# Performance work log

Hardware: AMD Instinct MI355X
Metric: run time of the kernel (lower is better)

The kernel has to match this reference:

```python
import jax, jax.numpy as jnp
import numpy as np

H = 1024   # hidden_size
NH = 16    # num_heads
HD = H // NH
B, S = 2, 2048


def setup_inputs() -> dict:
    key = jax.random.key(0)
    ks = jax.random.split(key, 6)
    std = 0.02
    x = jax.random.normal(ks[0], (B, S, H), dtype=jnp.float32)
    w_qkv = jax.random.normal(ks[1], (3 * H, H), dtype=jnp.float32) * std
    b_qkv = jnp.zeros((3 * H,), dtype=jnp.float32)
    ln_g = jnp.ones((H,), dtype=jnp.float32)
    ln_b = jnp.zeros((H,), dtype=jnp.float32)
    w_ent = jax.random.normal(ks[2], (1, H), dtype=jnp.float32) * std
    b_ent = jnp.zeros((1,), dtype=jnp.float32)
    w_out = jax.random.normal(ks[3], (H, H), dtype=jnp.float32) * std
    b_out = jnp.zeros((H,), dtype=jnp.float32)
    return {"x": x, "ln_g": ln_g, "ln_b": ln_b, "w_qkv": w_qkv, "b_qkv": b_qkv,
            "w_ent": w_ent, "b_ent": b_ent, "w_out": w_out, "b_out": b_out}


def reference(x, ln_g, ln_b, w_qkv, b_qkv, w_ent, b_ent, w_out, b_out):
    b, s, h = x.shape
    scale = 1.0 / jnp.sqrt(jnp.float32(HD))
    TEMP = 0.1  # fixed softmax temperature

    # LayerNorm (eps=1e-6)
    mu = jnp.mean(x, axis=-1, keepdims=True)
    var = jnp.mean(jnp.square(x - mu), axis=-1, keepdims=True)
    xn = (x - mu) / jnp.sqrt(var + 1e-6) * ln_g + ln_b

    # QKV projection -> [B, S, 3, NH, HD] -> q,k,v each [B, NH, S, HD]
    qkv = xn @ w_qkv.T + b_qkv
    qkv = qkv.reshape(b, s, 3, NH, HD).transpose(2, 0, 3, 1, 4)
    q, k, v = qkv[0], qkv[1], qkv[2]

    # Scaled causal scores [B, NH, S, S]
    scores = jnp.einsum('bhqd,bhkd->bhqk', q, k) * scale
    causal = jnp.tril(jnp.ones((s, s), dtype=bool))
    scores = jnp.where(causal[None, None], scores, -jnp.inf)

    # Sharpened softmax (temperature 0.1); dropout is identity in eval
    probs = jax.nn.softmax(scores / TEMP, axis=-1)

    # Entropy gate over keys: sigmoid proj on post-LN x, clamped [0.1, 2.0]
    gate = jax.nn.sigmoid(xn @ w_ent.T + b_ent)        # [B, S, 1]
    gate = jnp.clip(gate, 0.1, 2.0)[:, None, None, :, 0]  # [B, 1, 1, S]
    probs = probs * gate

    # Weighted values -> merge heads -> output projection, scaled by 0.1
    out = jnp.einsum('bhqk,bhkd->bhqd', probs, v)
    out = out.transpose(0, 2, 1, 3).reshape(b, s, h)
    return (out @ w_out.T + b_out) * 0.1
```

## Files before the change

### kernel.cpp

```cpp
#include <hip/hip_runtime.h>

typedef __bf16 bf16x8 __attribute__((ext_vector_type(8)));
typedef float floatx4 __attribute__((ext_vector_type(4)));
typedef unsigned short u16;

#define LOG2E 1.44269504088896340736f
#define BF16_ONE 0x3F80u

static __device__ __forceinline__ float bf2f(u16 u) {
  union { unsigned int i; float f; } c; c.i = ((unsigned int)u) << 16; return c.f;
}
static __device__ __forceinline__ u16 f2bf(float f) {
  union { float f; unsigned int i; } c; c.f = f;
  unsigned int x = c.i;
  unsigned int r = (x >> 16) & 1u;
  x += 0x7fffu + r;
  return (u16)(x >> 16);
}
static __device__ __forceinline__ u16 f2bf_rne(float f) {
  __bf16 h = (__bf16)f;
  union { __bf16 h; u16 u; } c; c.h = h; return c.u;
}
static __device__ __forceinline__ float fast_exp2(float x) {
#if __has_builtin(__builtin_amdgcn_exp2f)
  return __builtin_amdgcn_exp2f(x);
#else
  return exp2f(x);
#endif
}
static __device__ __forceinline__ float ldp(const void* p, int i, bool isbf) {
  return isbf ? bf2f(((const u16*)p)[i]) : ((const float*)p)[i];
}

static __device__ __forceinline__ float blockSum(float v, float* red, int wave, int lane) {
  #pragma unroll
  for (int o = 32; o > 0; o >>= 1) v += __shfl_xor(v, o);
  __syncthreads();
  if (lane == 0) red[wave] = v;
  __syncthreads();
  return red[0] + red[1] + red[2] + red[3];
}

__global__ __launch_bounds__(256) void prep_kernel(
    const void* __restrict__ w_qkv, u16* __restrict__ w_qkv_c,
    const void* __restrict__ w_out, u16* __restrict__ w_out_c,
    const void* __restrict__ x, const void* __restrict__ g, const void* __restrict__ bta,
    const void* __restrict__ w_ent, const void* __restrict__ b_ent,
    u16* __restrict__ xn, float* __restrict__ gate, const u16* __restrict__ probe)
{
  __shared__ float red[4];
  bool isbf = (probe[0] == BF16_ONE);
  int blk = blockIdx.x;
  int tid = threadIdx.x;

  if (blk < 2048) {
    int i = blk * 256 + tid;
    const void* src = w_qkv; u16* dst = w_qkv_c;
    if (i >= 393216) { i -= 393216; src = w_out; dst = w_out_c; }
    if (isbf) {
      ((uint4*)dst)[i] = ((const uint4*)src)[i];
    } else {
      const float4* s = (const float4*)src;
      float4 a = s[2 * i], b = s[2 * i + 1];
      u16 o[8] = {f2bf(a.x), f2bf(a.y), f2bf(a.z), f2bf(a.w),
                  f2bf(b.x), f2bf(b.y), f2bf(b.z), f2bf(b.w)};
      *(uint4*)(&dst[8 * i]) = *(uint4*)o;
    }
    return;
  }

  int row = blk - 2048;
  int wave = tid >> 6, lane = tid & 63;

  float v[4];
  #pragma unroll
  for (int i = 0; i < 4; ++i) {
    size_t idx = (size_t)row * 1024 + tid + 256 * i;
    v[i] = isbf ? bf2f(((const u16*)x)[idx]) : ((const float*)x)[idx];
  }

  float mu = blockSum(v[0] + v[1] + v[2] + v[3], red, wave, lane) * (1.0f / 1024.0f);

  float vs = 0.f;
  #pragma unroll
  for (int i = 0; i < 4; ++i) { float d = v[i] - mu; vs += d * d; }
  float var = blockSum(vs, red, wave, lane) * (1.0f / 1024.0f);
  float rstd = rsqrtf(var + 1e-6f);

  float gp = 0.f;
  #pragma unroll
  for (int i = 0; i < 4; ++i) {
    int col = tid + 256 * i;
    float xv = (v[i] - mu) * rstd * ldp(g, col, isbf) + ldp(bta, col, isbf);
    xn[(size_t)row * 1024 + col] = f2bf(xv);
    gp += xv * ldp(w_ent, col, isbf);
  }
  float tot = blockSum(gp, red, wave, lane);
  if (tid == 0) {
    float z = tot + ldp(b_ent, 0, isbf);
    float sg = 1.0f / (1.0f + exp2f(-z * LOG2E));
    gate[row] = fminf(fmaxf(sg, 0.1f), 2.0f);
  }
}

#define GEMM_STAGE(Abase, Wbase) \
  { \
    int lrow = lane >> 3; \
    int scb = ((lane & 7) ^ lrow) * 8; \
    _Pragma("unroll") \
    for (int it = 0; it < 4; ++it) { \
      int chunk = wave * 4 + it; \
      int row = chunk * 8 + lrow; \
      __builtin_amdgcn_global_load_lds( \
        (const __attribute__((address_space(1))) void*)&Abase[(size_t)(m0 + row) * K + k0 + scb], \
        (__attribute__((address_space(3))) void*)&As[chunk * 512], 16, 0, 0); \
      __builtin_amdgcn_global_load_lds( \
        (const __attribute__((address_space(1))) void*)&Wbase[(size_t)(n0 + row) * K + k0 + scb], \
        (__attribute__((address_space(3))) void*)&Ws[chunk * 512], 16, 0, 0); \
    } \
  }

#define GEMM_COMPUTE() \
  _Pragma("unroll") \
  for (int kk = 0; kk < 64; kk += 32) { \
    int kkb = kk >> 3; \
    bf16x8 af[4], bfr[4]; \
    _Pragma("unroll") \
    for (int i = 0; i < 4; ++i) \
      af[i] = *(const bf16x8*)(&As[(wm + 16 * i + lr) * 64 + ((kkb + lg) ^ (lr & 7)) * 8]); \
    _Pragma("unroll") \
    for (int j = 0; j < 4; ++j) \
      bfr[j] = *(const bf16x8*)(&Ws[(wn + 16 * j + lr) * 64 + ((kkb + lg) ^ (lr & 7)) * 8]); \
    _Pragma("unroll") \
    for (int i = 0; i < 4; ++i) \
      _Pragma("unroll") \
      for (int j = 0; j < 4; ++j) \
        acc[i][j] = __builtin_amdgcn_mfma_f32_16x16x32_bf16(af[i], bfr[j], acc[i][j], 0, 0, 0); \
  }

__global__ __launch_bounds__(256) void gemm_bt_kernel(
    const u16* __restrict__ A, const u16* __restrict__ W, const void* __restrict__ bias,
    const float* __restrict__ gate, u16* __restrict__ C, int M, int N, int K,
    const u16* __restrict__ probe)
{
  __shared__ __align__(16) u16 As[128 * 64];
  __shared__ __align__(16) u16 Ws[128 * 64];
  int m0 = blockIdx.y * 128, n0 = blockIdx.x * 128;
  int tid = threadIdx.x, wave = tid >> 6, lane = tid & 63;
  int lr = lane & 15, lg = lane >> 4;
  int wm = (wave >> 1) * 64, wn = (wave & 1) * 64;

  floatx4 acc[4][4];
  #pragma unroll
  for (int i = 0; i < 4; ++i)
    #pragma unroll
    for (int j = 0; j < 4; ++j)
      #pragma unroll
      for (int r = 0; r < 4; ++r) acc[i][j][r] = 0.f;

  for (int k0 = 0; k0 < K; k0 += 64) {
    GEMM_STAGE(A, W)
    __syncthreads();
    GEMM_COMPUTE()
    __syncthreads();
  }

  bool isbf = (probe[0] == BF16_ONE);
  bool doGate = (n0 >= 2048);
  float gm[4][4];
  #pragma unroll
  for (int i = 0; i < 4; ++i)
    #pragma unroll
    for (int r = 0; r < 4; ++r)
      gm[i][r] = doGate ? gate[m0 + wm + 16 * i + lg * 4 + r] : 1.0f;

  #pragma unroll
  for (int j = 0; j < 4; ++j) {
    int n = n0 + wn + 16 * j + lr;
    float bv = ldp(bias, n, isbf);
    #pragma unroll
    for (int i = 0; i < 4; ++i) {
      int mbase = m0 + wm + 16 * i + lg * 4;
      #pragma unroll
      for (int r = 0; r < 4; ++r)
        C[(size_t)(mbase + r) * N + n] = f2bf((acc[i][j][r] + bv) * gm[i][r]);
    }
  }
}

__global__ __launch_bounds__(256) void gemm_out_kernel(
    const u16* __restrict__ A, const u16* __restrict__ W, const void* __restrict__ bias,
    void* __restrict__ C, int M, int N, int K, float scale, const u16* __restrict__ probe)
{
  __shared__ __align__(16) u16 As[64 * 64];
  __shared__ __align__(16) u16 Ws[128 * 64];
  int m0 = blockIdx.y * 64, n0 = blockIdx.x * 128;
  int tid = threadIdx.x, wave = tid >> 6, lane = tid & 63;
  int lr = lane & 15, lg = lane >> 4;
  int wn = wave * 32;

  floatx4 acc[4][2];
  #pragma unroll
  for (int i = 0; i < 4; ++i)
    #pragma unroll
    for (int j = 0; j < 2; ++j)
      #pragma unroll
      for (int r = 0; r < 4; ++r) acc[i][j][r] = 0.f;

  for (int k0 = 0; k0 < K; k0 += 64) {
    {
      int lrow = lane >> 3;
      int scb = ((lane & 7) ^ lrow) * 8;
      #pragma unroll
      for (int c = wave; c < 24; c += 4) {
        if (c < 8) {
          int row = c * 8 + lrow;
          __builtin_amdgcn_global_load_lds(
            (const __attribute__((address_space(1))) void*)&A[(size_t)(m0 + row) * K + k0 + scb],
            (__attribute__((address_space(3))) void*)&As[c * 512], 16, 0, 0);
        } else {
          int cc = c - 8;
          int row = cc * 8 + lrow;
          __builtin_amdgcn_global_load_lds(
            (const __attribute__((address_space(1))) void*)&W[(size_t)(n0 + row) * K + k0 + scb],
            (__attribute__((address_space(3))) void*)&Ws[cc * 512], 16, 0, 0);
        }
      }
    }
    __syncthreads();
    #pragma unroll
    for (int kk = 0; kk < 64; kk += 32) {
      int kkb = kk >> 3;
      bf16x8 af[4], bfr[2];
      #pragma unroll
      for (int i = 0; i < 4; ++i)
        af[i] = *(const bf16x8*)(&As[(16 * i + lr) * 64 + ((kkb + lg) ^ (lr & 7)) * 8]);
      #pragma unroll
      for (int j = 0; j < 2; ++j)
        bfr[j] = *(const bf16x8*)(&Ws[(wn + 16 * j + lr) * 64 + ((kkb + lg) ^ (lr & 7)) * 8]);
      #pragma unroll
      for (int i = 0; i < 4; ++i)
        #pragma unroll
        for (int j = 0; j < 2; ++j)
          acc[i][j] = __builtin_amdgcn_mfma_f32_16x16x32_bf16(af[i], bfr[j], acc[i][j], 0, 0, 0);
    }
    __syncthreads();
  }

  bool isbf = (probe[0] == BF16_ONE);
  #pragma unroll
  for (int j = 0; j < 2; ++j) {
    int n = n0 + wn + 16 * j + lr;
    float bv = ldp(bias, n, isbf);
    #pragma unroll
    for (int i = 0; i < 4; ++i) {
      int mbase = m0 + 16 * i + lg * 4;
      #pragma unroll
      for (int r = 0; r < 4; ++r) {
        float v = (acc[i][j][r] + bv) * scale;
        size_t idx = (size_t)(mbase + r) * N + n;
        if (isbf) ((u16*)C)[idx] = f2bf(v);
        else      ((float*)C)[idx] = v;
      }
    }
  }
}

#define PSTR 72
#define CEXP (1.25f * LOG2E)

__global__ __launch_bounds__(512, 4) void attn_kernel(
    const u16* __restrict__ qkv, u16* __restrict__ out)
{
  __shared__ __align__(16) u16 Ks[2][64 * 72];
  __shared__ __align__(16) u16 Vt[2][64 * 72];
  __shared__ __align__(16) u16 Ps[8][16 * PSTR];

  int bid = blockIdx.x;
  int xcd = bid & 7, kb = bid >> 3;
  int bh = xcd * 4 + (kb >> 4);
  int pr = kb & 15;
  int h = bh & 15, b = bh >> 4;
  int tid = threadIdx.x, wave = tid >> 6, lane = tid & 63;
  int lr = lane & 15, lg = lane >> 4;
  const int RS = 3072;

  int tA = pr, tB = 31 - pr;
  bool isA = (wave >= 4);
  int wv = wave & 3;
  int myT = isA ? tA : tB;

  bf16x8 qf[2];
  int qrb = b * 2048 + myT * 64 + wv * 16;
  #pragma unroll
  for (int kk = 0; kk < 2; ++kk)
    qf[kk] = *(const bf16x8*)(&qkv[(size_t)(qrb + lr) * RS + h * 64 + kk * 32 + lg * 8]);

  floatx4 accO[4];
  float l = 0.f;
  #pragma unroll
  for (int jt = 0; jt < 4; ++jt)
    #pragma unroll
    for (int r = 0; r < 4; ++r) accO[jt][r] = 0.f;

  u16* ps = Ps[wave];

  int srow = tid >> 3, sc8 = (tid & 7) * 8;
  int kq = tid & 31, dg = tid >> 5;
  uint4 kp;
  uint2 vv0, vv1;

  auto LOADKV = [&](int kt) {
    int krow0 = b * 2048 + kt * 64;
    kp = *(const uint4*)(&qkv[(size_t)(krow0 + srow) * RS + 1024 + h * 64 + sc8]);
    const u16* vbp = &qkv[(size_t)krow0 * RS + 2048 + h * 64];
    vv0 = *(const uint2*)(&vbp[(size_t)(2 * kq) * RS + 4 * dg]);
    vv1 = *(const uint2*)(&vbp[(size_t)(2 * kq + 1) * RS + 4 * dg]);
  };
  auto COMMIT = [&](int bi) {
    *(uint4*)(&Ks[bi][srow * 72 + sc8]) = kp;
    #pragma unroll
    for (int d = 0; d < 4; ++d) {
      unsigned w0 = (&vv0.x)[d >> 1], w1 = (&vv1.x)[d >> 1];
      unsigned e0 = (d & 1) ? (w0 >> 16) : (w0 & 0xffffu);
      unsigned e1 = (d & 1) ? (w1 >> 16) : (w1 & 0xffffu);
      *(unsigned*)(&Vt[bi][(4 * dg + d) * 72 + 2 * kq]) = e0 | (e1 << 16);
    }
  };

  LOADKV(0);
  COMMIT(0);
  LOADKV(1);
  __syncthreads();

  int qg = wv * 16 + lr;
  for (int kt = 0; kt <= tB; ++kt) {
    int cur = kt & 1;
    if (!isA || kt <= tA) {
      bool diag = (kt == myT);
      const u16* ks = Ks[cur];
      const u16* vt = Vt[cur];
      #pragma unroll
      for (int jt = 0; jt < 4; ++jt) {
        floatx4 a = {0.f, 0.f, 0.f, 0.f};
        #pragma unroll
        for (int kk = 0; kk < 2; ++kk) {
          bf16x8 bk = *(const bf16x8*)(&ks[(jt * 16 + lr) * 72 + kk * 32 + lg * 8]);
          a = __builtin_amdgcn_mfma_f32_16x16x32_bf16(bk, qf[kk], a, 0, 0, 0);
        }
        int kbase = jt * 16 + lg * 4;
        u16 pb[4];
        #pragma unroll
        for (int r = 0; r < 4; ++r) {
          float e = fast_exp2(a[r] * CEXP);
          if (diag && (kbase + r) > qg) e = 0.f;
          l += e;
          pb[r] = f2bf_rne(e);
        }
        *(uint2*)(&ps[lr * PSTR + kbase]) = *(uint2*)pb;
      }
      bf16x8 ap[2];
      #pragma unroll
      for (int kk = 0; kk < 2; ++kk)
        ap[kk] = *(const bf16x8*)(&ps[lr * PSTR + kk * 32 + lg * 8]);
      #pragma unroll
      for (int jt = 0; jt < 4; ++jt)
        #pragma unroll
        for (int kk = 0; kk < 2; ++kk) {
          bf16x8 bv = *(const bf16x8*)(&vt[(jt * 16 + lr) * 72 + kk * 32 + lg * 8]);
          accO[jt] = __builtin_amdgcn_mfma_f32_16x16x32_bf16(ap[kk], bv, accO[jt], 0, 0, 0);
        }
    }
    if (kt < tB) {
      COMMIT(cur ^ 1);
      if (kt + 2 <= tB) LOADKV(kt + 2);
      __syncthreads();
    }
  }

  l += __shfl_xor(l, 16); l += __shfl_xor(l, 32);
  float li[4];
  #pragma unroll
  for (int r = 0; r < 4; ++r)
    li[r] = 1.0f / fmaxf(__shfl(l, lg * 4 + r), 1e-30f);
  #pragma unroll
  for (int jt = 0; jt < 4; ++jt)
    #pragma unroll
    for (int r = 0; r < 4; ++r) {
      int m = qrb + lg * 4 + r;
      out[(size_t)m * 1024 + h * 64 + jt * 16 + lr] = f2bf(accO[jt][r] * li[r]);
    }
}

extern "C" void kernel_launch(void* const* d_in, const int* in_sizes, int n_in,
                              void* d_out, int out_size, void* d_ws, size_t ws_size,
                              hipStream_t stream) {
  const void* x     = d_in[0];
  const void* ln_g  = d_in[1];
  const void* ln_b  = d_in[2];
  const void* w_qkv = d_in[3];
  const void* b_qkv = d_in[4];
  const void* w_ent = d_in[5];
  const void* b_ent = d_in[6];
  const void* w_out = d_in[7];
  const void* b_out = d_in[8];
  const u16* probe = (const u16*)ln_g;

  char* ws = (char*)d_ws;
  float* gate    = (float*)(ws);
  u16* xc        = (u16*)(ws + (64u << 10));
  u16* qkvb      = (u16*)(ws + (64u << 10) + (8u << 20));
  u16* w_qkv_c   = (u16*)(ws + (64u << 10) + (32u << 20));
  u16* w_out_c   = (u16*)(ws + (64u << 10) + (38u << 20));

  prep_kernel<<<6144, 256, 0, stream>>>(w_qkv, w_qkv_c, w_out, w_out_c,
                                        x, ln_g, ln_b, w_ent, b_ent, xc, gate, probe);
  gemm_bt_kernel<<<dim3(24, 32), 256, 0, stream>>>(xc, w_qkv_c, b_qkv, gate, qkvb, 4096, 3072, 1024, probe);
  attn_kernel<<<512, 512, 0, stream>>>(qkvb, xc );
  gemm_out_kernel<<<dim3(8, 64), 256, 0, stream>>>(xc, w_out_c, b_out, d_out, 4096, 1024, 1024, 0.1f, probe);
}
```

Baseline: 199.0 us.

## Retile QKV GEMM to 128x192 with 512 threads and skip bf16 weight copy

The QKV projection GEMM now uses 128x192 tiles across 8 waves, with each wave computing a 64x48 sub-tile. This gives 512 blocks, which should fill the CUs more evenly than the old 768 blocks of 128x128. When inputs are already bf16, the prep kernel skips copying the weights and both GEMMs read the original weight buffers directly. The gate multiply is now chosen per 16-column sub-tile, because a 192-wide tile can straddle the V boundary at 2048.

```diff
diff --git a/kernel.cpp b/kernel.cpp
--- a/kernel.cpp
+++ b/kernel.cpp
@@ -54,18 +54,15 @@
   int tid = threadIdx.x;
 
   if (blk < 2048) {
+    if (isbf) return;
     int i = blk * 256 + tid;
     const void* src = w_qkv; u16* dst = w_qkv_c;
     if (i >= 393216) { i -= 393216; src = w_out; dst = w_out_c; }
-    if (isbf) {
-      ((uint4*)dst)[i] = ((const uint4*)src)[i];
-    } else {
-      const float4* s = (const float4*)src;
-      float4 a = s[2 * i], b = s[2 * i + 1];
-      u16 o[8] = {f2bf(a.x), f2bf(a.y), f2bf(a.z), f2bf(a.w),
-                  f2bf(b.x), f2bf(b.y), f2bf(b.z), f2bf(b.w)};
-      *(uint4*)(&dst[8 * i]) = *(uint4*)o;
-    }
+    const float4* s = (const float4*)src;
+    float4 a = s[2 * i], b = s[2 * i + 1];
+    u16 o[8] = {f2bf(a.x), f2bf(a.y), f2bf(a.z), f2bf(a.w),
+                f2bf(b.x), f2bf(b.y), f2bf(b.z), f2bf(b.w)};
+    *(uint4*)(&dst[8 * i]) = *(uint4*)o;
     return;
   }
 
@@ -103,97 +100,104 @@
   }
 }
 
-#define GEMM_STAGE(Abase, Wbase) \
-  { \
-    int lrow = lane >> 3; \
-    int scb = ((lane & 7) ^ lrow) * 8; \
-    _Pragma("unroll") \
-    for (int it = 0; it < 4; ++it) { \
-      int chunk = wave * 4 + it; \
-      int row = chunk * 8 + lrow; \
-      __builtin_amdgcn_global_load_lds( \
-        (const __attribute__((address_space(1))) void*)&Abase[(size_t)(m0 + row) * K + k0 + scb], \
-        (__attribute__((address_space(3))) void*)&As[chunk * 512], 16, 0, 0); \
-      __builtin_amdgcn_global_load_lds( \
-        (const __attribute__((address_space(1))) void*)&Wbase[(size_t)(n0 + row) * K + k0 + scb], \
-        (__attribute__((address_space(3))) void*)&Ws[chunk * 512], 16, 0, 0); \
-    } \
-  }
-
-#define GEMM_COMPUTE() \
-  _Pragma("unroll") \
-  for (int kk = 0; kk < 64; kk += 32) { \
-    int kkb = kk >> 3; \
-    bf16x8 af[4], bfr[4]; \
-    _Pragma("unroll") \
-    for (int i = 0; i < 4; ++i) \
-      af[i] = *(const bf16x8*)(&As[(wm + 16 * i + lr) * 64 + ((kkb + lg) ^ (lr & 7)) * 8]); \
-    _Pragma("unroll") \
-    for (int j = 0; j < 4; ++j) \
-      bfr[j] = *(const bf16x8*)(&Ws[(wn + 16 * j + lr) * 64 + ((kkb + lg) ^ (lr & 7)) * 8]); \
-    _Pragma("unroll") \
-    for (int i = 0; i < 4; ++i) \
-      _Pragma("unroll") \
-      for (int j = 0; j < 4; ++j) \
-        acc[i][j] = __builtin_amdgcn_mfma_f32_16x16x32_bf16(af[i], bfr[j], acc[i][j], 0, 0, 0); \
-  }
-
-__global__ __launch_bounds__(256) void gemm_bt_kernel(
-    const u16* __restrict__ A, const u16* __restrict__ W, const void* __restrict__ bias,
-    const float* __restrict__ gate, u16* __restrict__ C, int M, int N, int K,
+__global__ __launch_bounds__(512, 4) void gemm_qkv_kernel(
+    const u16* __restrict__ A, const void* __restrict__ Wf, const u16* __restrict__ Wc,
+    const void* __restrict__ bias, const float* __restrict__ gate, u16* __restrict__ C,
     const u16* __restrict__ probe)
 {
   __shared__ __align__(16) u16 As[128 * 64];
-  __shared__ __align__(16) u16 Ws[128 * 64];
-  int m0 = blockIdx.y * 128, n0 = blockIdx.x * 128;
+  __shared__ __align__(16) u16 Ws[192 * 64];
+  const int K = 1024, N = 3072;
+  bool isbf = (probe[0] == BF16_ONE);
+  const u16* W = isbf ? (const u16*)Wf : Wc;
+
+  int bid = blockIdx.x;
+  int n0 = (bid & 15) * 192, m0 = (bid >> 4) * 128;
   int tid = threadIdx.x, wave = tid >> 6, lane = tid & 63;
   int lr = lane & 15, lg = lane >> 4;
-  int wm = (wave >> 1) * 64, wn = (wave & 1) * 64;
-
-  floatx4 acc[4][4];
+  int wm = (wave >> 2) * 64, wn = (wave & 3) * 48;
+  int lrow = lane >> 3;
+  int scb = ((lane & 7) ^ lrow) * 8;
+
+  floatx4 acc[4][3];
   #pragma unroll
   for (int i = 0; i < 4; ++i)
     #pragma unroll
-    for (int j = 0; j < 4; ++j)
+    for (int j = 0; j < 3; ++j)
       #pragma unroll
       for (int r = 0; r < 4; ++r) acc[i][j][r] = 0.f;
 
   for (int k0 = 0; k0 < K; k0 += 64) {
-    GEMM_STAGE(A, W)
+    #pragma unroll
+    for (int it = 0; it < 5; ++it) {
+      int c = wave + it * 8;
+      if (c < 16) {
+        int row = c * 8 + lrow;
+        __builtin_amdgcn_global_load_lds(
+          (const __attribute__((address_space(1))) void*)&A[(size_t)(m0 + row) * K + k0 + scb],
+          (__attribute__((address_space(3))) void*)&As[c * 512], 16, 0, 0);
+      } else {
+        int cc = c - 16;
+        int row = cc * 8 + lrow;
+        __builtin_amdgcn_global_load_lds(
+          (const __attribute__((address_space(1))) void*)&W[(size_t)(n0 + row) * K + k0 + scb],
+          (__attribute__((address_space(3))) void*)&Ws[cc * 512], 16, 0, 0);
+      }
+    }
     __syncthreads();
-    GEMM_COMPUTE()
+    #pragma unroll
+    for (int kk = 0; kk < 64; kk += 32) {
+      int kkb = kk >> 3;
+      bf16x8 af[4], bfr[3];
+      #pragma unroll
+      for (int i = 0; i < 4; ++i)
+        af[i] = *(const bf16x8*)(&As[(wm + 16 * i + lr) * 64 + ((kkb + lg) ^ (lr & 7)) * 8]);
+      #pragma unroll
+      for (int j = 0; j < 3; ++j)
+        bfr[j] = *(const bf16x8*)(&Ws[(wn + 16 * j + lr) * 64 + ((kkb + lg) ^ (lr & 7)) * 8]);
+      #pragma unroll
+      for (int i = 0; i < 4; ++i)
+        #pragma unroll
+        for (int j = 0; j < 3; ++j)
+          acc[i][j] = __builtin_amdgcn_mfma_f32_16x16x32_bf16(af[i], bfr[j], acc[i][j], 0, 0, 0);
+    }
     __syncthreads();
   }
 
-  bool isbf = (probe[0] == BF16_ONE);
-  bool doGate = (n0 >= 2048);
-  float gm[4][4];
+  float gv[4][4];
   #pragma unroll
   for (int i = 0; i < 4; ++i)
     #pragma unroll
     for (int r = 0; r < 4; ++r)
-      gm[i][r] = doGate ? gate[m0 + wm + 16 * i + lg * 4 + r] : 1.0f;
-
-  #pragma unroll
-  for (int j = 0; j < 4; ++j) {
+      gv[i][r] = gate[m0 + wm + 16 * i + lg * 4 + r];
+
+  #pragma unroll
+  for (int j = 0; j < 3; ++j) {
     int n = n0 + wn + 16 * j + lr;
+    bool dg = (n0 + wn + 16 * j) >= 2048;
     float bv = ldp(bias, n, isbf);
     #pragma unroll
     for (int i = 0; i < 4; ++i) {
       int mbase = m0 + wm + 16 * i + lg * 4;
       #pragma unroll
-      for (int r = 0; r < 4; ++r)
-        C[(size_t)(mbase + r) * N + n] = f2bf((acc[i][j][r] + bv) * gm[i][r]);
+      for (int r = 0; r < 4; ++r) {
+        float val = acc[i][j][r] + bv;
+        if (dg) val *= gv[i][r];
+        C[(size_t)(mbase + r) * N + n] = f2bf(val);
+      }
     }
   }
 }
 
 __global__ __launch_bounds__(256) void gemm_out_kernel(
-    const u16* __restrict__ A, const u16* __restrict__ W, const void* __restrict__ bias,
+    const u16* __restrict__ A, const void* __restrict__ Wf, const u16* __restrict__ Wc,
+    const void* __restrict__ bias,
     void* __restrict__ C, int M, int N, int K, float scale, const u16* __restrict__ probe)
 {
   __shared__ __align__(16) u16 As[64 * 64];
   __shared__ __align__(16) u16 Ws[128 * 64];
+  bool isbf = (probe[0] == BF16_ONE);
+  const u16* W = isbf ? (const u16*)Wf : Wc;
   int m0 = blockIdx.y * 64, n0 = blockIdx.x * 128;
   int tid = threadIdx.x, wave = tid >> 6, lane = tid & 63;
   int lr = lane & 15, lg = lane >> 4;
@@ -247,7 +251,6 @@
     __syncthreads();
   }
 
-  bool isbf = (probe[0] == BF16_ONE);
   #pragma unroll
   for (int j = 0; j < 2; ++j) {
     int n = n0 + wn + 16 * j + lr;
@@ -415,7 +418,8 @@
 
   prep_kernel<<<6144, 256, 0, stream>>>(w_qkv, w_qkv_c, w_out, w_out_c,
                                         x, ln_g, ln_b, w_ent, b_ent, xc, gate, probe);
-  gemm_bt_kernel<<<dim3(24, 32), 256, 0, stream>>>(xc, w_qkv_c, b_qkv, gate, qkvb, 4096, 3072, 1024, probe);
+  gemm_qkv_kernel<<<512, 512, 0, stream>>>(xc, w_qkv, w_qkv_c, b_qkv, gate, qkvb, probe);
   attn_kernel<<<512, 512, 0, stream>>>(qkvb, xc );
-  gemm_out_kernel<<<dim3(8, 64), 256, 0, stream>>>(xc, w_out_c, b_out, d_out, 4096, 1024, 1024, 0.1f, probe);
-}
+  gemm_out_kernel<<<dim3(8, 64), 256, 0, stream>>>(xc, w_out, w_out_c, b_out, d_out,
+                                                   4096, 1024, 1024, 0.1f, probe);
+}
```

Result: faster. 185.3 us (-6.9%).
